# Kernel optimization log

Hardware: AMD Instinct MI355X
Metric: run time of the kernel (lower is better)

The kernel has to match this reference:

```python
import jax, jax.numpy as jnp
import numpy as np

NUM_HEAD = 8
HIDDEN = 128
INPUT_DIM = 256
N1 = 1024
N2 = 1024
BATCH = 16


def setup_inputs() -> dict:
    key = jax.random.key(0)
    ks = jax.random.split(key, 10)
    HD = HIDDEN * NUM_HEAD  # 1024
    return {
        "x1": jax.random.normal(ks[0], (BATCH, N1, INPUT_DIM), jnp.float32),
        "x2": jax.random.normal(ks[1], (BATCH, N2, INPUT_DIM), jnp.float32),
        "B": jax.random.normal(ks[2], (N1, N2), jnp.float32),
        "wq_w": jax.random.normal(ks[3], (HD, INPUT_DIM), jnp.float32) * 0.02,
        "wq_b": jnp.zeros((HD,), jnp.float32),
        "wk_w": jax.random.normal(ks[4], (HD, INPUT_DIM), jnp.float32) * 0.02,
        "wk_b": jnp.zeros((HD,), jnp.float32),
        "wv_w": jax.random.normal(ks[5], (HD, INPUT_DIM), jnp.float32) * 0.02,
        "wv_b": jnp.zeros((HD,), jnp.float32),
        "proj_w": jax.random.normal(ks[6], (HIDDEN, HD), jnp.float32) * 0.02,
        "proj_b": jnp.zeros((HIDDEN,), jnp.float32),
    }


def reference(x1, x2, B, wq_w, wq_b, wk_w, wk_b, wv_w, wv_b, proj_w, proj_b):
    b, n1, _ = x1.shape
    n2 = x2.shape[1]
    sdk = jnp.sqrt(jnp.asarray(HIDDEN, x1.dtype))
    # Linear layers (torch convention: y = x @ W.T + b)
    q = x1 @ wq_w.T + wq_b                      # [b, n1, H*D]
    k = x2 @ wk_w.T + wk_b                      # [b, n2, H*D]
    v = x2 @ wv_w.T + wv_b                      # [b, n2, H*D]
    q = q.reshape(b, n1, NUM_HEAD, HIDDEN)
    k = k.reshape(b, n2, NUM_HEAD, HIDDEN)
    v = v.reshape(b, n2, NUM_HEAD, HIDDEN)
    # scores: [b, h, n1, n2]
    scores = jnp.einsum("bnhd,bmhd->bhnm", q, k) / sdk + B[None, None, :, :]
    attn = jax.nn.softmax(scores, axis=-1)
    out = jnp.einsum("bhnm,bmhd->bnhd", attn, v).reshape(b, n1, NUM_HEAD * HIDDEN)
    return out @ proj_w.T + proj_b              # [b, n1, HIDDEN]
```

## Files before the change

kernel.cpp:

```cpp
#include <hip/hip_runtime.h>
#include <hip/hip_fp16.h>

typedef _Float16 f16;
typedef __attribute__((ext_vector_type(4))) _Float16 f16x4;
typedef __attribute__((ext_vector_type(8))) _Float16 f16x8;
typedef __attribute__((ext_vector_type(4))) float f32x4;

#define MFMA_F16(a,b,c) __builtin_amdgcn_mfma_f32_16x16x32_f16((a),(b),(c),0,0,0)

__device__ __forceinline__ void gl_lds16(const f16* g, f16* l) {
  __builtin_amdgcn_global_load_lds(
      (const __attribute__((address_space(1))) unsigned int*)g,
      (__attribute__((address_space(3))) unsigned int*)l, 16, 0, 0);
}


__global__ __launch_bounds__(256) void conv_pack(
    const float* __restrict__ x1, const float* __restrict__ x2,
    const float* __restrict__ wq, const float* __restrict__ wk,
    const float* __restrict__ wv,
    f16* __restrict__ x1p, f16* __restrict__ x2p, f16* __restrict__ wp) {
  __shared__ f16 S[128][264];
  const int id = blockIdx.x, tid = threadIdx.x;
  const float* src;
  f16* dst;
  if (id < 128) {
    src = x1 + (size_t)id * 32768; dst = x1p + (size_t)id * 32768;
  } else if (id < 256) {
    src = x2 + (size_t)(id - 128) * 32768; dst = x2p + (size_t)(id - 128) * 32768;
  } else {
    const int wsel = (id - 256) >> 3, wt = (id - 256) & 7;
    const float* wsrc = (wsel == 0) ? wq : (wsel == 1) ? wk : wv;
    src = wsrc + (size_t)wt * 32768;
    dst = wp + (size_t)wsel * 262144 + (size_t)wt * 32768;
  }
#pragma unroll 8
  for (int i = 0; i < 32; i++) {
    int f = i * 256 + tid;
    int row = f >> 6, c4 = f & 63;
    float4 v = *(const float4*)(src + (size_t)row * 256 + c4 * 4);
    f16x4 hh; hh[0] = (f16)v.x; hh[1] = (f16)v.y; hh[2] = (f16)v.z; hh[3] = (f16)v.w;
    *(f16x4*)&S[row][c4 * 4] = hh;
  }
  __syncthreads();
#pragma unroll 8
  for (int i = 0; i < 16; i++) {
    int u = i * 256 + tid;
    int chunk = u >> 6, l2 = u & 63;
    int q = l2 >> 4, c = l2 & 15;
    int row = (chunk >> 3) * 16 + c, k = (chunk & 7) * 32 + q * 8;
    f16x8 v = *(const f16x8*)&S[row][k];
    *(f16x8*)(dst + (size_t)u * 8) = v;
  }
}

__global__ __launch_bounds__(512) __attribute__((amdgpu_waves_per_eu(4, 4)))
void gemm_qkv(const f16* __restrict__ x1p, const f16* __restrict__ x2p,
              const f16* __restrict__ wp,
              const float* __restrict__ wqb, const float* __restrict__ wkb,
              const float* __restrict__ wvb,
              f16* __restrict__ Qp, f16* __restrict__ Kp, f16* __restrict__ Vp,
              float qscale) {
  __shared__ f16 Wl[2][8192];
  __shared__ f16 Xl[2][8192];
  const int z = blockIdx.z;
  const f16* Xp = (z == 0) ? x1p : x2p;
  const float* bias = (z == 0) ? wqb : (z == 1) ? wkb : wvb;
  f16* outp = (z == 0) ? Qp : (z == 1) ? Kp : Vp;
  const float sc = (z == 0) ? qscale : 1.0f;

  const int tid = threadIdx.x, lane = tid & 63, wid = tid >> 6;
  const int col = lane & 15, quad = lane >> 4;
  const int xt = blockIdx.x, h = blockIdx.y;
  const int wr = wid >> 2, xc = wid & 3;
  const f16* Xb = Xp + (size_t)xt * 32768;
  const f16* Wb = wp + (size_t)z * 262144 + (size_t)h * 32768;

#define QISSUE(T, bufi)                                                   \
  {                                                                       \
    _Pragma("unroll") for (int j = 0; j < 2; j++) {                       \
      int lc = wid * 2 + j;                                               \
      int rt = lc >> 1, ksl = lc & 1;                                     \
      gl_lds16(Wb + (size_t)((rt * 8 + (T) * 2 + ksl) << 9) + lane * 8,   \
               &Wl[bufi][lc * 512]);                                      \
      gl_lds16(Xb + (size_t)((rt * 8 + (T) * 2 + ksl) << 9) + lane * 8,   \
               &Xl[bufi][lc * 512]);                                      \
    }                                                                     \
  }

  QISSUE(0, 0);
  QISSUE(1, 1);

  f32x4 acc[4][2];
#pragma unroll
  for (int i = 0; i < 4; i++)
#pragma unroll
    for (int j = 0; j < 2; j++) acc[i][j] = (f32x4){0.f, 0.f, 0.f, 0.f};

  __syncthreads();

  for (int t = 0; t < 4; ++t) {
    const int buf = t & 1;
    const f16* Ra = (z == 2) ? Xl[buf] : Wl[buf];
    const f16* Cb = (z == 2) ? Wl[buf] : Xl[buf];
#pragma unroll
    for (int ksl = 0; ksl < 2; ksl++) {
      f16x8 af[4], bf[2];
#pragma unroll
      for (int i = 0; i < 4; i++)
        af[i] = *(const f16x8*)&Ra[((wr * 4 + i) * 2 + ksl) * 512 + lane * 8];
#pragma unroll
      for (int j = 0; j < 2; j++)
        bf[j] = *(const f16x8*)&Cb[((xc * 2 + j) * 2 + ksl) * 512 + lane * 8];
#pragma unroll
      for (int i = 0; i < 4; i++)
#pragma unroll
        for (int j = 0; j < 2; j++) acc[i][j] = MFMA_F16(af[i], bf[j], acc[i][j]);
    }
    __syncthreads();
    if (t + 2 < 4) QISSUE(t + 2, buf);
  }

  if (z < 2) {
#pragma unroll
    for (int i = 0; i < 4; i++) {
      const int k0h = wr * 64 + i * 16 + quad * 4;
      float4 bq = *(const float4*)(bias + h * 128 + k0h);
      const int ks2 = k0h >> 5, q2 = (k0h >> 3) & 3, lo = k0h & 7;
#pragma unroll
      for (int j = 0; j < 2; j++) {
        const int bn2 = xt * 128 + xc * 32 + j * 16 + col;
        const int b = bn2 >> 10, n2 = bn2 & 1023;
        const int T = n2 >> 6, jt = (n2 >> 4) & 3, c2 = n2 & 15;
        f16x4 pk;
#pragma unroll
        for (int r = 0; r < 4; r++)
          pk[r] = (f16)((acc[i][j][r] + ((const float*)&bq)[r]) * sc);
        *(f16x4*)(outp + (size_t)(b * 8 + h) * 131072 + T * 8192 +
                  (jt * 4 + ks2) * 512 + (q2 * 16 + c2) * 8 + lo) = pk;
      }
    }
  } else {
#pragma unroll
    for (int j = 0; j < 2; j++) {
      const int d = xc * 32 + j * 16 + col;
      const float bv = bias[h * 128 + d];
      const int ct = d >> 4, cc = d & 15;
#pragma unroll
      for (int i = 0; i < 4; i++) {
        const int bn2 = xt * 128 + wr * 64 + i * 16 + quad * 4;
        const int b = bn2 >> 10, n2 = bn2 & 1023;
        const int T = n2 >> 6, kv6 = n2 & 63;
        const int ks2 = kv6 >> 5, qv = (kv6 >> 3) & 3, jj = kv6 & 7;
        f16x4 pk;
#pragma unroll
        for (int r = 0; r < 4; r++) pk[r] = (f16)(acc[i][j][r] + bv);
        *(f16x4*)(outp + (size_t)(b * 8 + h) * 131072 + T * 8192 +
                  (ct * 2 + ks2) * 512 + (qv * 16 + cc) * 8 + jj) = pk;
      }
    }
  }
}

__global__ __launch_bounds__(256) void gemm_proj(const f16* __restrict__ A,
                                                 const float* __restrict__ W,
                                                 const float* __restrict__ bias,
                                                 float* __restrict__ out) {
  constexpr int LD = 72;
  __shared__ f16 As[64][LD];
  __shared__ f16 Bs[64][LD];
  const int tid = threadIdx.x, lane = tid & 63, wid = tid >> 6;
  const int col = lane & 15, quad = lane >> 4;
  const int wm = (wid >> 1) * 32, wn = (wid & 1) * 32;
  const int m0 = blockIdx.x * 64, n0 = blockIdx.y * 64;

  f32x4 acc[2][2];
#pragma unroll
  for (int i = 0; i < 2; i++)
#pragma unroll
    for (int j = 0; j < 2; j++) acc[i][j] = (f32x4){0.f, 0.f, 0.f, 0.f};

  for (int kt = 0; kt < 16; ++kt) {
    const int k0 = kt * 64;
#pragma unroll
    for (int i = 0; i < 2; i++) {
      int f = i * 256 + tid;
      int r = f >> 3, ch = f & 7;
      *(f16x8*)&As[r][ch * 8] = *(const f16x8*)(A + (size_t)(m0 + r) * 1024 + k0 + ch * 8);
    }
#pragma unroll
    for (int i = 0; i < 4; i++) {
      int f = i * 256 + tid;
      int r = f >> 4, c4 = f & 15;
      float4 v = *(const float4*)(W + (size_t)(n0 + r) * 1024 + k0 + c4 * 4);
      f16x4 hh; hh[0] = (f16)v.x; hh[1] = (f16)v.y; hh[2] = (f16)v.z; hh[3] = (f16)v.w;
      *(f16x4*)&Bs[r][c4 * 4] = hh;
    }
    __syncthreads();
#pragma unroll
    for (int ks = 0; ks < 2; ks++) {
      f16x8 af[2], bf[2];
#pragma unroll
      for (int i = 0; i < 2; i++) af[i] = *(const f16x8*)&As[wm + i * 16 + col][ks * 32 + quad * 8];
#pragma unroll
      for (int j = 0; j < 2; j++) bf[j] = *(const f16x8*)&Bs[wn + j * 16 + col][ks * 32 + quad * 8];
#pragma unroll
      for (int i = 0; i < 2; i++)
#pragma unroll
        for (int j = 0; j < 2; j++) acc[i][j] = MFMA_F16(af[i], bf[j], acc[i][j]);
    }
    __syncthreads();
  }
#pragma unroll
  for (int j = 0; j < 2; j++) {
    const int c = n0 + wn + j * 16 + col;
    const float bv = bias[c];
#pragma unroll
    for (int i = 0; i < 2; i++) {
      const int r0 = m0 + wm + i * 16 + quad * 4;
#pragma unroll
      for (int r = 0; r < 4; r++)
        out[(size_t)(r0 + r) * 128 + c] = acc[i][j][r] + bv;
    }
  }
}

__global__ __launch_bounds__(512) __attribute__((amdgpu_waves_per_eu(4, 4)))
void attn_fused(const f16* __restrict__ Qp, const f16* __restrict__ Kp,
                const f16* __restrict__ Vp, const float* __restrict__ Bm,
                f16* __restrict__ O) {
  __shared__ f16 Ksl[2][8192];
  __shared__ f16 Vtl[2][8192];
  __shared__ f16 Ps[8192];
  const int tid = threadIdx.x, lane = tid & 63, wid = tid >> 6;
  const int col = lane & 15, quad = lane >> 4;
  const int id = blockIdx.x;
  const int mt = (id >> 3) & 7;
  const int bh = ((id >> 6) << 3) | (id & 7);
  const int b = bh >> 3, h = bh & 7;
  const int m0 = mt * 128;
  const int wm = wid * 16;

  const f16* Qb = Qp + (size_t)bh * 131072;
  const f16* Kb = Kp + (size_t)bh * 131072;
  const f16* Vb = Vp + (size_t)bh * 131072;

#define AISSUE(T, bufi)                                                       \
  {                                                                           \
    if (wid < 4) {                                                            \
      _Pragma("unroll") for (int j = 0; j < 4; j++)                           \
          gl_lds16(Kb + (size_t)(T) * 8192 + (wid * 4 + j) * 512 + lane * 8,  \
                   &Ksl[bufi][(wid * 4 + j) * 512]);                          \
    } else {                                                                  \
      _Pragma("unroll") for (int j = 0; j < 4; j++)                           \
          gl_lds16(Vb + (size_t)(T) * 8192 + ((wid - 4) * 4 + j) * 512 + lane * 8, \
                   &Vtl[bufi][((wid - 4) * 4 + j) * 512]);                    \
    }                                                                         \
  }

  AISSUE(0, 0);
  AISSUE(1, 1);

  f16x8 qf[4];
  {
    const int m = m0 + wm;
    const int T = m >> 6, jt2 = (m >> 4) & 3;
#pragma unroll
    for (int ks = 0; ks < 4; ks++)
      qf[ks] = *(const f16x8*)(Qb + T * 8192 + (jt2 * 4 + ks) * 512 + lane * 8);
  }

  f32x4 oacc[8];
  float l = 0.f;
#pragma unroll
  for (int ct = 0; ct < 8; ct++) oacc[ct] = (f32x4){0.f, 0.f, 0.f, 0.f};

  __syncthreads();

  for (int t = 0; t < 16; ++t) {
    const int buf = t & 1;
    const int n0 = t * 64;

    float4 breg[4];
    {
      const float* Brow = Bm + (size_t)(m0 + wm + col) * 1024 + n0;
#pragma unroll
      for (int jt = 0; jt < 4; jt++)
        breg[jt] = *(const float4*)(Brow + jt * 16 + quad * 4);
    }

    f32x4 s[4];
#pragma unroll
    for (int jt = 0; jt < 4; jt++) s[jt] = (f32x4){0.f, 0.f, 0.f, 0.f};
#pragma unroll
    for (int ks = 0; ks < 4; ks++) {
      f16x8 kf[4];
#pragma unroll
      for (int jt = 0; jt < 4; jt++)
        kf[jt] = *(const f16x8*)&Ksl[buf][(jt * 4 + ks) * 512 + lane * 8];
#pragma unroll
      for (int jt = 0; jt < 4; jt++) s[jt] = MFMA_F16(kf[jt], qf[ks], s[jt]);
    }

    {
      const int m = wm + col;
#pragma unroll
      for (int jt = 0; jt < 4; jt++) {
        const float* bv = (const float*)&breg[jt];
        float p0 = __expf(s[jt][0] + bv[0]);
        float p1 = __expf(s[jt][1] + bv[1]);
        float p2 = __expf(s[jt][2] + bv[2]);
        float p3 = __expf(s[jt][3] + bv[3]);
        l += (p0 + p1) + (p2 + p3);
        f16x4 pk; pk[0] = (f16)p0; pk[1] = (f16)p1; pk[2] = (f16)p2; pk[3] = (f16)p3;
        const int g = (jt * 2 + (quad >> 1)) ^ (col & 7);
        *(f16x4*)&Ps[m * 64 + g * 8 + (quad & 1) * 4] = pk;
      }
    }

#pragma unroll
    for (int ks = 0; ks < 2; ks++) {
      const int m = wm + col;
      const int g = (ks * 4 + quad) ^ (col & 7);
      f16x8 pf = *(const f16x8*)&Ps[m * 64 + g * 8];
#pragma unroll
      for (int ct = 0; ct < 8; ct++) {
        f16x8 vf = *(const f16x8*)&Vtl[buf][(ct * 2 + ks) * 512 + lane * 8];
        oacc[ct] = MFMA_F16(pf, vf, oacc[ct]);
      }
    }

    __syncthreads();
    if (t + 2 < 16) AISSUE(t + 2, buf);
  }

  l += __shfl_xor(l, 16);
  l += __shfl_xor(l, 32);
  f16* Ob = O + ((size_t)(b * 1024 + m0 + wm)) * 1024 + h * 128;
#pragma unroll
  for (int r = 0; r < 4; r++) {
    const float lv = __shfl(l, (lane & 48) | (quad * 4 + r));
    const float inv = 1.0f / lv;
#pragma unroll
    for (int ct = 0; ct < 8; ct++)
      Ob[(size_t)(quad * 4 + r) * 1024 + ct * 16 + col] = (f16)(oacc[ct][r] * inv);
  }
}

extern "C" void kernel_launch(void* const* d_in, const int* in_sizes, int n_in,
                              void* d_out, int out_size, void* d_ws, size_t ws_size,
                              hipStream_t stream) {
  (void)in_sizes; (void)n_in; (void)out_size; (void)ws_size;
  const float* x1  = (const float*)d_in[0];
  const float* x2  = (const float*)d_in[1];
  const float* Bm  = (const float*)d_in[2];
  const float* wq  = (const float*)d_in[3];
  const float* wqb = (const float*)d_in[4];
  const float* wk  = (const float*)d_in[5];
  const float* wkb = (const float*)d_in[6];
  const float* wv  = (const float*)d_in[7];
  const float* wvb = (const float*)d_in[8];
  const float* pw  = (const float*)d_in[9];
  const float* pb  = (const float*)d_in[10];
  float* out = (float*)d_out;

  const size_t MiB = 1024 * 1024;
  f16* Qp  = (f16*)d_ws;
  f16* Kp  = (f16*)((char*)d_ws + 32 * MiB);
  f16* Vp  = (f16*)((char*)d_ws + 64 * MiB);
  f16* Ow  = (f16*)((char*)d_ws + 96 * MiB);
  f16* x1p = (f16*)((char*)d_ws + 96 * MiB);
  f16* x2p = (f16*)((char*)d_ws + 104 * MiB);
  f16* wp  = (f16*)((char*)d_ws + 112 * MiB);

  const float scale = 0.0883883476483184f;
  conv_pack<<<dim3(280), dim3(256), 0, stream>>>(x1, x2, wq, wk, wv, x1p, x2p, wp);
  gemm_qkv<<<dim3(128, 8, 3), dim3(512), 0, stream>>>(x1p, x2p, wp, wqb, wkb, wvb,
                                                      Qp, Kp, Vp, scale);
  attn_fused<<<dim3(1024), dim3(512), 0, stream>>>(Qp, Kp, Vp, Bm, Ow);
  gemm_proj<<<dim3(256, 2), dim3(256), 0, stream>>>(Ow, pw, pb, out);
}
```

Measured before the change: 279.0 us.

## Software-pipeline QK scores one tile ahead of softmax and PV

Splits the K and V async LDS loads into separate issue macros and prefetches K one tile further ahead than V. It computes the QK^T scores for tile t+1 while tile t's exp/softmax and PV MFMAs run, swapping two score register sets across a 2x-unrolled loop. The aim is to overlap the score MFMAs with the exp work and the LDS traffic, shortening the dependency chain in each iteration. In exchange it uses more registers for the second score set and fully unrolls the loop into a larger body.

```diff
diff --git a/kernel.cpp b/kernel.cpp
--- a/kernel.cpp
+++ b/kernel.cpp
@@ -245,21 +245,23 @@
   const f16* Kb = Kp + (size_t)bh * 131072;
   const f16* Vb = Vp + (size_t)bh * 131072;
 
-#define AISSUE(T, bufi)                                                       \
-  {                                                                           \
-    if (wid < 4) {                                                            \
-      _Pragma("unroll") for (int j = 0; j < 4; j++)                           \
-          gl_lds16(Kb + (size_t)(T) * 8192 + (wid * 4 + j) * 512 + lane * 8,  \
-                   &Ksl[bufi][(wid * 4 + j) * 512]);                          \
-    } else {                                                                  \
-      _Pragma("unroll") for (int j = 0; j < 4; j++)                           \
-          gl_lds16(Vb + (size_t)(T) * 8192 + ((wid - 4) * 4 + j) * 512 + lane * 8, \
-                   &Vtl[bufi][((wid - 4) * 4 + j) * 512]);                    \
-    }                                                                         \
-  }
-
-  AISSUE(0, 0);
-  AISSUE(1, 1);
+#define ISSUE_K(T, bufi)                                                      \
+  if (wid < 4) {                                                              \
+    _Pragma("unroll") for (int j = 0; j < 4; j++)                             \
+        gl_lds16(Kb + (size_t)(T) * 8192 + (wid * 4 + j) * 512 + lane * 8,    \
+                 &Ksl[bufi][(wid * 4 + j) * 512]);                            \
+  }
+#define ISSUE_V(T, bufi)                                                      \
+  if (wid >= 4) {                                                             \
+    _Pragma("unroll") for (int j = 0; j < 4; j++)                             \
+        gl_lds16(Vb + (size_t)(T) * 8192 + ((wid - 4) * 4 + j) * 512 + lane * 8, \
+                 &Vtl[bufi][((wid - 4) * 4 + j) * 512]);                      \
+  }
+
+  ISSUE_K(0, 0);
+  ISSUE_K(1, 1);
+  ISSUE_V(0, 0);
+  ISSUE_V(1, 1);
 
   f16x8 qf[4];
   {
@@ -275,63 +277,78 @@
 #pragma unroll
   for (int ct = 0; ct < 8; ct++) oacc[ct] = (f32x4){0.f, 0.f, 0.f, 0.f};
 
+  f32x4 sA[4], sB[4];
+
   __syncthreads();
 
-  for (int t = 0; t < 16; ++t) {
-    const int buf = t & 1;
-    const int n0 = t * 64;
-
-    float4 breg[4];
-    {
-      const float* Brow = Bm + (size_t)(m0 + wm + col) * 1024 + n0;
-#pragma unroll
-      for (int jt = 0; jt < 4; jt++)
-        breg[jt] = *(const float4*)(Brow + jt * 16 + quad * 4);
-    }
-
-    f32x4 s[4];
-#pragma unroll
-    for (int jt = 0; jt < 4; jt++) s[jt] = (f32x4){0.f, 0.f, 0.f, 0.f};
-#pragma unroll
-    for (int ks = 0; ks < 4; ks++) {
-      f16x8 kf[4];
-#pragma unroll
-      for (int jt = 0; jt < 4; jt++)
-        kf[jt] = *(const f16x8*)&Ksl[buf][(jt * 4 + ks) * 512 + lane * 8];
-#pragma unroll
-      for (int jt = 0; jt < 4; jt++) s[jt] = MFMA_F16(kf[jt], qf[ks], s[jt]);
-    }
-
-    {
-      const int m = wm + col;
-#pragma unroll
-      for (int jt = 0; jt < 4; jt++) {
-        const float* bv = (const float*)&breg[jt];
-        float p0 = __expf(s[jt][0] + bv[0]);
-        float p1 = __expf(s[jt][1] + bv[1]);
-        float p2 = __expf(s[jt][2] + bv[2]);
-        float p3 = __expf(s[jt][3] + bv[3]);
-        l += (p0 + p1) + (p2 + p3);
-        f16x4 pk; pk[0] = (f16)p0; pk[1] = (f16)p1; pk[2] = (f16)p2; pk[3] = (f16)p3;
-        const int g = (jt * 2 + (quad >> 1)) ^ (col & 7);
-        *(f16x4*)&Ps[m * 64 + g * 8 + (quad & 1) * 4] = pk;
-      }
-    }
-
-#pragma unroll
-    for (int ks = 0; ks < 2; ks++) {
-      const int m = wm + col;
-      const int g = (ks * 4 + quad) ^ (col & 7);
-      f16x8 pf = *(const f16x8*)&Ps[m * 64 + g * 8];
-#pragma unroll
-      for (int ct = 0; ct < 8; ct++) {
-        f16x8 vf = *(const f16x8*)&Vtl[buf][(ct * 2 + ks) * 512 + lane * 8];
-        oacc[ct] = MFMA_F16(pf, vf, oacc[ct]);
-      }
-    }
-
-    __syncthreads();
-    if (t + 2 < 16) AISSUE(t + 2, buf);
+#pragma unroll
+  for (int jt = 0; jt < 4; jt++) sA[jt] = (f32x4){0.f, 0.f, 0.f, 0.f};
+#pragma unroll
+  for (int ks = 0; ks < 4; ks++) {
+    f16x8 kf[4];
+#pragma unroll
+    for (int jt = 0; jt < 4; jt++)
+      kf[jt] = *(const f16x8*)&Ksl[0][(jt * 4 + ks) * 512 + lane * 8];
+#pragma unroll
+    for (int jt = 0; jt < 4; jt++) sA[jt] = MFMA_F16(kf[jt], qf[ks], sA[jt]);
+  }
+  __syncthreads();
+  ISSUE_K(2, 0);
+
+#define BODY(t, SC, SN)                                                        \
+  {                                                                            \
+    const int n0 = (t) * 64;                                                   \
+    float4 breg[4];                                                            \
+    {                                                                          \
+      const float* Brow = Bm + (size_t)(m0 + wm + col) * 1024 + n0;            \
+      _Pragma("unroll") for (int jt = 0; jt < 4; jt++)                         \
+          breg[jt] = *(const float4*)(Brow + jt * 16 + quad * 4);              \
+    }                                                                          \
+    if ((t) < 15) {                                                            \
+      _Pragma("unroll") for (int jt = 0; jt < 4; jt++)                         \
+          SN[jt] = (f32x4){0.f, 0.f, 0.f, 0.f};                                \
+      _Pragma("unroll") for (int ks = 0; ks < 4; ks++) {                       \
+        f16x8 kf[4];                                                           \
+        _Pragma("unroll") for (int jt = 0; jt < 4; jt++)                       \
+            kf[jt] = *(const f16x8*)&Ksl[((t) + 1) & 1]                        \
+                         [(jt * 4 + ks) * 512 + lane * 8];                     \
+        _Pragma("unroll") for (int jt = 0; jt < 4; jt++)                       \
+            SN[jt] = MFMA_F16(kf[jt], qf[ks], SN[jt]);                         \
+      }                                                                        \
+    }                                                                          \
+    {                                                                          \
+      const int m = wm + col;                                                  \
+      _Pragma("unroll") for (int jt = 0; jt < 4; jt++) {                       \
+        const float* bv = (const float*)&breg[jt];                             \
+        float p0 = __expf(SC[jt][0] + bv[0]);                                  \
+        float p1 = __expf(SC[jt][1] + bv[1]);                                  \
+        float p2 = __expf(SC[jt][2] + bv[2]);                                  \
+        float p3 = __expf(SC[jt][3] + bv[3]);                                  \
+        l += (p0 + p1) + (p2 + p3);                                            \
+        f16x4 pk; pk[0] = (f16)p0; pk[1] = (f16)p1;                            \
+        pk[2] = (f16)p2; pk[3] = (f16)p3;                                      \
+        const int g = (jt * 2 + (quad >> 1)) ^ (col & 7);                      \
+        *(f16x4*)&Ps[m * 64 + g * 8 + (quad & 1) * 4] = pk;                    \
+      }                                                                        \
+    }                                                                          \
+    _Pragma("unroll") for (int ks = 0; ks < 2; ks++) {                         \
+      const int m = wm + col;                                                  \
+      const int g = (ks * 4 + quad) ^ (col & 7);                               \
+      f16x8 pf = *(const f16x8*)&Ps[m * 64 + g * 8];                           \
+      _Pragma("unroll") for (int ct = 0; ct < 8; ct++) {                       \
+        f16x8 vf = *(const f16x8*)&Vtl[(t) & 1][(ct * 2 + ks) * 512 + lane * 8]; \
+        oacc[ct] = MFMA_F16(pf, vf, oacc[ct]);                                 \
+      }                                                                        \
+    }                                                                          \
+    __syncthreads();                                                           \
+    if ((t) + 3 < 16) ISSUE_K((t) + 3, ((t) + 3) & 1);                         \
+    if ((t) + 2 < 16) ISSUE_V((t) + 2, (t) & 1);                               \
+  }
+
+#pragma unroll
+  for (int tt = 0; tt < 16; tt += 2) {
+    BODY(tt, sA, sB);
+    BODY(tt + 1, sB, sA);
   }
 
   l += __shfl_xor(l, 16);
```

Result: slower. 520.2 us (+86.4%).
